# Performance work log

Measured on AMD Instinct MI355X. Metric: run time of the kernel, lower is better.

The kernel has to match this reference:

```python
import jax, jax.numpy as jnp
import numpy as np

B, S, E, H, D, RD = 1, 2048, 2560, 32, 80, 32  # batch, seq, n_embd, heads, head_dim, rotary_dim


def setup_inputs() -> dict:
    key = jax.random.key(0)
    k0, k1, k2 = jax.random.split(key, 3)
    hidden_states = jax.random.normal(k0, (B, S, E), dtype=jnp.float32)
    Wqkv_w = jax.random.normal(k1, (3 * E, E), dtype=jnp.float32) * 0.02
    Wqkv_b = jnp.zeros((3 * E,), dtype=jnp.float32)
    out_w = jax.random.normal(k2, (E, E), dtype=jnp.float32) * 0.02
    out_b = jnp.zeros((E,), dtype=jnp.float32)
    # RotaryEmbedding tables: inv_freq over even indices of rotary_dim
    inv_freq = 1.0 / (10000.0 ** (jnp.arange(0, RD, 2, dtype=jnp.float32) / RD))  # [RD/2]
    t = jnp.arange(S, dtype=jnp.float32)
    freqs = t[:, None] * inv_freq[None, :]  # [S, RD/2]
    return {
        "hidden_states": hidden_states,
        "Wqkv_w": Wqkv_w,
        "Wqkv_b": Wqkv_b,
        "out_w": out_w,
        "out_b": out_b,
        "cos": jnp.cos(freqs),
        "sin": jnp.sin(freqs),
    }


def _apply_rotary(x, cos, sin):
    # x: [B, S, H, D]; rotate first 2*cos.shape[-1] dims (GPT-NeoX half-split style)
    rd = cos.shape[-1] * 2
    x_rot, x_pass = x[..., :rd], x[..., rd:]
    x1, x2 = jnp.split(x_rot, 2, axis=-1)
    c = cos[None, :, None, :]  # [1, S, 1, rd/2]
    s = sin[None, :, None, :]
    rotated = jnp.concatenate([x1 * c - x2 * s, x1 * s + x2 * c], axis=-1)
    return jnp.concatenate([rotated, x_pass], axis=-1)


def reference(hidden_states, Wqkv_w, Wqkv_b, out_w, out_b, cos, sin):
    b, s, e = hidden_states.shape
    qkv = hidden_states @ Wqkv_w.T + Wqkv_b              # [B, S, 3E]
    qkv = qkv.reshape(b, s, 3, H, D)
    q = _apply_rotary(qkv[:, :, 0], cos[:s], sin[:s])    # [B, S, H, D]
    k = _apply_rotary(qkv[:, :, 1], cos[:s], sin[:s])
    v = qkv[:, :, 2]
    scale = 1.0 / np.sqrt(D).astype(np.float32)
    scores = jnp.einsum("bthd,bshd->bhts", q, k) * scale  # [B, H, S, S]
    causal = jnp.triu(jnp.full((s, s), -10000.0, dtype=scores.dtype), 1)
    scores = scores + causal
    attn = jax.nn.softmax(scores, axis=-1)
    out = jnp.einsum("bhts,bshd->bthd", attn, v).reshape(b, s, H * D)
    return out @ out_w.T + out_b
```

## Files before the change

### kernel.cpp

```cpp
#include <hip/hip_runtime.h>
#include <hip/hip_bf16.h>

typedef __attribute__((ext_vector_type(8))) __bf16 bf16x8;
typedef __attribute__((ext_vector_type(8))) short s16x8;
typedef __attribute__((ext_vector_type(4))) float f32x4;
typedef unsigned short u16;
typedef unsigned int u32;

static __device__ __forceinline__ float bf2f(u16 u) {
  union { unsigned int i; float f; } x;
  x.i = ((unsigned int)u) << 16;
  return x.f;
}
static __device__ __forceinline__ u16 f2bf(float f) {
  __hip_bfloat16 h = __float2bfloat16(f);
  return __builtin_bit_cast(u16, h);
}

__global__ void cvt3_kernel(const float* __restrict__ s0, u16* __restrict__ d0, int n0,
                            const float* __restrict__ s1, u16* __restrict__ d1, int n1,
                            const float* __restrict__ s2, u16* __restrict__ d2, int n2) {
  const int stride = gridDim.x * blockDim.x;
  const int t0 = blockIdx.x * blockDim.x + threadIdx.x;
  for (int i = t0; i < n0; i += stride) {
    float4 f = reinterpret_cast<const float4*>(s0)[i];
    ushort4 u{f2bf(f.x), f2bf(f.y), f2bf(f.z), f2bf(f.w)};
    reinterpret_cast<ushort4*>(d0)[i] = u;
  }
  for (int i = t0; i < n1; i += stride) {
    float4 f = reinterpret_cast<const float4*>(s1)[i];
    ushort4 u{f2bf(f.x), f2bf(f.y), f2bf(f.z), f2bf(f.w)};
    reinterpret_cast<ushort4*>(d1)[i] = u;
  }
  for (int i = t0; i < n2; i += stride) {
    float4 f = reinterpret_cast<const float4*>(s2)[i];
    ushort4 u{f2bf(f.x), f2bf(f.y), f2bf(f.z), f2bf(f.w)};
    reinterpret_cast<ushort4*>(d2)[i] = u;
  }
}

template <typename OUT_T>
__global__ __launch_bounds__(512, 2) void gemm256_bt(
    const u16* __restrict__ A, const u16* __restrict__ B,
    const float* __restrict__ bias, OUT_T* __restrict__ C,
    int M, int N, int K) {
  __shared__ u16 As[2][256 * 64];
  __shared__ u16 Bs[2][256 * 64];
  const int tid = threadIdx.x;
  const int w = tid >> 6;
  const int lane = tid & 63;
  const int g = lane >> 4, c = lane & 15;
  const int wm = w >> 2, wn = w & 3;
  const int nwg = gridDim.x * gridDim.y;
  const int flat = blockIdx.y * gridDim.x + blockIdx.x;
  const int swz = (flat & 7) * (nwg >> 3) + (flat >> 3);
  const int bx = swz % gridDim.x, by = swz / gridDim.x;
  const int row0 = by * 256, col0 = bx * 256;
  const int nt = K >> 6;

  f32x4 acc[8][4] = {};

  auto issue = [&](const u16* __restrict__ base, int rb, int t, u16* lds) {
#pragma unroll
    for (int rr = 0; rr < 4; ++rr) {
      int q = rr * 512 + tid;
      int r = q >> 3;
      int cl = (q & 7) ^ (r & 7);
      const u16* gp = base + (size_t)(rb + r) * K + (t << 6) + cl * 8;
      __builtin_amdgcn_global_load_lds(
          (const __attribute__((address_space(1))) void*)gp,
          (__attribute__((address_space(3))) void*)(lds + q * 8), 16, 0, 0);
    }
  };

  issue(A, row0, 0, As[0]);
  issue(B, col0, 0, Bs[0]);

  int cur = 0;
  for (int t = 0; t < nt; ++t) {
    if (t + 1 < nt) {
      issue(A, row0, t + 1, As[cur ^ 1]);
      issue(B, col0, t + 1, Bs[cur ^ 1]);
      asm volatile("s_waitcnt vmcnt(8)" ::: "memory");
    } else {
      asm volatile("s_waitcnt vmcnt(0)" ::: "memory");
    }
    __builtin_amdgcn_s_barrier();

#pragma unroll
    for (int kk = 0; kk < 2; ++kk) {
      bf16x8 bfr[4], afr[8];
      const int p = (kk * 4 + g) ^ (c & 7);
#pragma unroll
      for (int nf = 0; nf < 4; ++nf) {
        int rowb = wn * 64 + nf * 16 + c;
        bfr[nf] = *reinterpret_cast<const bf16x8*>(&Bs[cur][(rowb * 8 + p) * 8]);
      }
#pragma unroll
      for (int mf = 0; mf < 8; ++mf) {
        int rowa = wm * 128 + mf * 16 + c;
        afr[mf] = *reinterpret_cast<const bf16x8*>(&As[cur][(rowa * 8 + p) * 8]);
      }
      __builtin_amdgcn_s_setprio(1);
#pragma unroll
      for (int mf = 0; mf < 8; ++mf)
#pragma unroll
        for (int nf = 0; nf < 4; ++nf)
          acc[mf][nf] = __builtin_amdgcn_mfma_f32_16x16x32_bf16(
              afr[mf], bfr[nf], acc[mf][nf], 0, 0, 0);
      __builtin_amdgcn_s_setprio(0);
    }
    __builtin_amdgcn_s_barrier();
    cur ^= 1;
  }

#pragma unroll
  for (int mf = 0; mf < 8; ++mf) {
#pragma unroll
    for (int nf = 0; nf < 4; ++nf) {
      int col = col0 + wn * 64 + nf * 16 + c;
      float bs = bias[col];
#pragma unroll
      for (int r = 0; r < 4; ++r) {
        int row = row0 + wm * 128 + mf * 16 + g * 4 + r;
        float v = acc[mf][nf][r] + bs;
        if constexpr (sizeof(OUT_T) == 2) {
          C[(size_t)row * N + col] = f2bf(v);
        } else {
          C[(size_t)row * N + col] = v;
        }
      }
    }
  }
}

template <typename OUT_T>
__global__ __launch_bounds__(256, 2) void gemm128p_bt(
    const u16* __restrict__ A, const u16* __restrict__ B,
    const float* __restrict__ bias, OUT_T* __restrict__ C,
    int M, int N, int K) {
  __shared__ u16 As[2][128 * 64];
  __shared__ u16 Bs[2][128 * 64];
  const int tid = threadIdx.x;
  const int w = tid >> 6;
  const int lane = tid & 63;
  const int g = lane >> 4, c = lane & 15;
  const int wm = w >> 1, wn = w & 1;
  const int nwg = gridDim.x * gridDim.y;
  const int flat = blockIdx.y * gridDim.x + blockIdx.x;
  const int swz = (flat & 7) * (nwg >> 3) + (flat >> 3);
  const int bx = swz % gridDim.x, by = swz / gridDim.x;
  const int row0 = by * 128, col0 = bx * 128;
  const int nt = K >> 6;

  f32x4 acc[4][4] = {};

  auto issue = [&](const u16* __restrict__ base, int rb, int t, u16* lds) {
#pragma unroll
    for (int rr = 0; rr < 4; ++rr) {
      int q = rr * 256 + tid;
      int r = q >> 3;
      int cl = (q & 7) ^ (r & 7);
      const u16* gp = base + (size_t)(rb + r) * K + (t << 6) + cl * 8;
      __builtin_amdgcn_global_load_lds(
          (const __attribute__((address_space(1))) void*)gp,
          (__attribute__((address_space(3))) void*)(lds + q * 8), 16, 0, 0);
    }
  };

  issue(A, row0, 0, As[0]);
  issue(B, col0, 0, Bs[0]);

  int cur = 0;
  for (int t = 0; t < nt; ++t) {
    if (t + 1 < nt) {
      issue(A, row0, t + 1, As[cur ^ 1]);
      issue(B, col0, t + 1, Bs[cur ^ 1]);
      asm volatile("s_waitcnt vmcnt(8)" ::: "memory");
    } else {
      asm volatile("s_waitcnt vmcnt(0)" ::: "memory");
    }
    __builtin_amdgcn_s_barrier();

#pragma unroll
    for (int kk = 0; kk < 2; ++kk) {
      bf16x8 afr[4], bfr[4];
      const int p = (kk * 4 + g) ^ (c & 7);
#pragma unroll
      for (int mi = 0; mi < 4; ++mi) {
        int rowa = wm * 64 + mi * 16 + c;
        afr[mi] = *reinterpret_cast<const bf16x8*>(&As[cur][(rowa * 8 + p) * 8]);
      }
#pragma unroll
      for (int ni = 0; ni < 4; ++ni) {
        int rowb = wn * 64 + ni * 16 + c;
        bfr[ni] = *reinterpret_cast<const bf16x8*>(&Bs[cur][(rowb * 8 + p) * 8]);
      }
      __builtin_amdgcn_s_setprio(1);
#pragma unroll
      for (int mi = 0; mi < 4; ++mi)
#pragma unroll
        for (int ni = 0; ni < 4; ++ni)
          acc[mi][ni] = __builtin_amdgcn_mfma_f32_16x16x32_bf16(
              afr[mi], bfr[ni], acc[mi][ni], 0, 0, 0);
      __builtin_amdgcn_s_setprio(0);
    }
    __builtin_amdgcn_s_barrier();
    cur ^= 1;
  }

#pragma unroll
  for (int mi = 0; mi < 4; ++mi) {
#pragma unroll
    for (int ni = 0; ni < 4; ++ni) {
      int col = col0 + wn * 64 + ni * 16 + c;
      float bs = bias[col];
#pragma unroll
      for (int r = 0; r < 4; ++r) {
        int row = row0 + wm * 64 + mi * 16 + g * 4 + r;
        float v = acc[mi][ni][r] + bs;
        if constexpr (sizeof(OUT_T) == 2) {
          C[(size_t)row * N + col] = f2bf(v);
        } else {
          C[(size_t)row * N + col] = v;
        }
      }
    }
  }
}

__global__ __launch_bounds__(256) void rope_kernel(
    const u16* __restrict__ qkv, const float* __restrict__ cosT,
    const float* __restrict__ sinT, u16* __restrict__ Qp, u16* __restrict__ Kp) {
  const int h = blockIdx.y;
  const int d = threadIdx.x & 127;
  const int sh = threadIdx.x >> 7;
  const float scale = 0.16129822f;
#pragma unroll
  for (int i = 0; i < 8; ++i) {
    const int s = blockIdx.x * 16 + i * 2 + sh;
    const size_t row = (size_t)s * 7680;
    if (d < 96) {
      float qo = 0.f, ko = 0.f;
      if (d < 80) {
        float q = bf2f(qkv[row + h * 80 + d]);
        float k = bf2f(qkv[row + 2560 + h * 80 + d]);
        if (d < 16) {
          float cs = cosT[s * 16 + d], sn = sinT[s * 16 + d];
          float q2 = bf2f(qkv[row + h * 80 + d + 16]);
          float k2 = bf2f(qkv[row + 2560 + h * 80 + d + 16]);
          qo = q * cs - q2 * sn;
          ko = k * cs - k2 * sn;
        } else if (d < 32) {
          float cs = cosT[s * 16 + d - 16], sn = sinT[s * 16 + d - 16];
          float q1 = bf2f(qkv[row + h * 80 + d - 16]);
          float k1 = bf2f(qkv[row + 2560 + h * 80 + d - 16]);
          qo = q1 * sn + q * cs;
          ko = k1 * sn + k * cs;
        } else {
          qo = q;
          ko = k;
        }
      }
      size_t o = ((size_t)h * 2048 + s) * 96 + d;
      Qp[o] = f2bf(qo * scale);
      Kp[o] = f2bf(ko);
    }
  }
}

__global__ __launch_bounds__(256) void vtrans_kernel(const u16* __restrict__ qkv,
                                                     u16* __restrict__ Vt) {
  __shared__ u16 Vs[80 * 136];
  const int tid = threadIdx.x;
  const int s0 = blockIdx.x * 128;
  const int h = blockIdx.y;
  const int s = tid >> 1;
  const int h2 = tid & 1;
#pragma unroll
  for (int j = 0; j < 5; ++j) {
    s16x8 v = *reinterpret_cast<const s16x8*>(
        &qkv[(size_t)(s0 + s) * 7680 + 5120 + h * 80 + h2 * 40 + j * 8]);
#pragma unroll
    for (int e = 0; e < 8; ++e)
      Vs[(h2 * 40 + j * 8 + e) * 136 + s] = (u16)v[e];
  }
  __syncthreads();
  for (int idx = tid; idx < 80 * 16; idx += 256) {
    int d = idx >> 4, s8 = idx & 15;
    s16x8 v = *reinterpret_cast<const s16x8*>(&Vs[d * 136 + s8 * 8]);
    *reinterpret_cast<s16x8*>(&Vt[((size_t)(h * 80 + d)) * 2048 + s0 + s8 * 8]) = v;
  }
}

__global__ __launch_bounds__(256, 2) void attn_kernel(
    const u16* __restrict__ Qp, const u16* __restrict__ Kp,
    const u16* __restrict__ Vt, u16* __restrict__ O) {
  __shared__ u32 Plds[4][32 * 36];
  __shared__ float mbuf[4][2][16];
  const int tid = threadIdx.x;
  const int w = tid >> 6;
  const int lane = tid & 63;
  const int g = lane >> 4, c = lane & 15;
  const int f = blockIdx.x;
  const int xcd = f & 7;
  const int k_ = f >> 3;
  const int h = (xcd << 2) | (k_ & 3);
  const int qb = 63 - (k_ >> 2);
  const int q0 = qb * 32;
  const size_t hq = (size_t)h * 2048;
  u32* Pw = &Plds[w][0];

  bf16x8 bq[2][3];
#pragma unroll
  for (int qi = 0; qi < 2; ++qi)
#pragma unroll
    for (int ch = 0; ch < 3; ++ch)
      bq[qi][ch] = *reinterpret_cast<const bf16x8*>(
          &Qp[(hq + q0 + qi * 16 + c) * 96 + ch * 32 + g * 8]);

  f32x4 accO[2][5] = {};
  float mrow[2] = {-1e30f, -1e30f};
  float lrow[2] = {0.f, 0.f};

  const int nkb = (q0 + 95) >> 6;
  for (int kbi = w; kbi < nkb; kbi += 4) {
    const int kb = kbi << 6;
    bf16x8 ak[4][3];
#pragma unroll
    for (int ki = 0; ki < 4; ++ki)
#pragma unroll
      for (int ch = 0; ch < 3; ++ch)
        ak[ki][ch] = *reinterpret_cast<const bf16x8*>(
            &Kp[(hq + kb + ki * 16 + c) * 96 + ch * 32 + g * 8]);
    bf16x8 av[5][2];
#pragma unroll
    for (int db = 0; db < 5; ++db)
#pragma unroll
      for (int kc = 0; kc < 2; ++kc)
        av[db][kc] = *reinterpret_cast<const bf16x8*>(
            &Vt[((size_t)h * 80 + db * 16 + c) * 2048 + kb + kc * 32 + g * 8]);

    f32x4 SS[4][2] = {};
    __builtin_amdgcn_s_setprio(1);
#pragma unroll
    for (int ch = 0; ch < 3; ++ch)
#pragma unroll
      for (int ki = 0; ki < 4; ++ki)
#pragma unroll
        for (int qi = 0; qi < 2; ++qi)
          SS[ki][qi] = __builtin_amdgcn_mfma_f32_16x16x32_bf16(
              ak[ki][ch], bq[qi][ch], SS[ki][qi], 0, 0, 0);
    __builtin_amdgcn_s_setprio(0);

    if (kbi == nkb - 1) {
#pragma unroll
      for (int ki = 0; ki < 4; ++ki)
#pragma unroll
        for (int qi = 0; qi < 2; ++qi)
#pragma unroll
          for (int r = 0; r < 4; ++r) {
            int k = kb + ki * 16 + g * 4 + r;
            int q = q0 + qi * 16 + c;
            if (k > q) SS[ki][qi][r] -= 14426.95f;
          }
    }

    float pmax[2];
    bool need = false;
#pragma unroll
    for (int qi = 0; qi < 2; ++qi) {
      float m2 = SS[0][qi][0];
#pragma unroll
      for (int ki = 0; ki < 4; ++ki)
#pragma unroll
        for (int r = 0; r < 4; ++r)
          if (ki | r) m2 = fmaxf(m2, SS[ki][qi][r]);
      m2 = fmaxf(m2, __shfl_xor(m2, 16));
      m2 = fmaxf(m2, __shfl_xor(m2, 32));
      pmax[qi] = m2;
      need = need || (m2 > mrow[qi] + 8.0f);
    }
    if (__any(need)) {
#pragma unroll
      for (int qi = 0; qi < 2; ++qi) {
        float mnew = fmaxf(mrow[qi], pmax[qi]);
        float sc = __builtin_amdgcn_exp2f(mrow[qi] - mnew);
        lrow[qi] *= sc;
#pragma unroll
        for (int db = 0; db < 5; ++db) accO[qi][db] *= sc;
        mrow[qi] = mnew;
      }
    }
#pragma unroll
    for (int qi = 0; qi < 2; ++qi) {
      float rs = 0.f;
#pragma unroll
      for (int ki = 0; ki < 4; ++ki)
#pragma unroll
        for (int r = 0; r < 4; ++r) {
          float pv = __builtin_amdgcn_exp2f(SS[ki][qi][r] - mrow[qi]);
          SS[ki][qi][r] = pv;
          rs += pv;
        }
      rs += __shfl_xor(rs, 16);
      rs += __shfl_xor(rs, 32);
      lrow[qi] += rs;
    }

#pragma unroll
    for (int qi = 0; qi < 2; ++qi)
#pragma unroll
      for (int ki = 0; ki < 4; ++ki)
#pragma unroll
        for (int r2 = 0; r2 < 2; ++r2) {
          u32 lo = f2bf(SS[ki][qi][r2 * 2]);
          u32 hi = f2bf(SS[ki][qi][r2 * 2 + 1]);
          Pw[(qi * 16 + c) * 36 + ki * 8 + g * 2 + r2] = lo | (hi << 16);
        }
    bf16x8 pa[2][2];
#pragma unroll
    for (int qi = 0; qi < 2; ++qi)
#pragma unroll
      for (int kc = 0; kc < 2; ++kc)
        pa[qi][kc] = *reinterpret_cast<const bf16x8*>(
            &Pw[(qi * 16 + c) * 36 + kc * 16 + g * 4]);

    __builtin_amdgcn_s_setprio(1);
#pragma unroll
    for (int kc = 0; kc < 2; ++kc)
#pragma unroll
      for (int db = 0; db < 5; ++db)
#pragma unroll
        for (int qi = 0; qi < 2; ++qi)
          accO[qi][db] = __builtin_amdgcn_mfma_f32_16x16x32_bf16(
              av[db][kc], pa[qi][kc], accO[qi][db], 0, 0, 0);
    __builtin_amdgcn_s_setprio(0);
  }

  mbuf[w][0][c] = mrow[0];
  mbuf[w][1][c] = mrow[1];
  __syncthreads();
#pragma unroll
  for (int qi = 0; qi < 2; ++qi) {
    float ms = fmaxf(fmaxf(mbuf[0][qi][c], mbuf[1][qi][c]),
                     fmaxf(mbuf[2][qi][c], mbuf[3][qi][c]));
    float fl = __builtin_amdgcn_exp2f(mrow[qi] - ms);
    lrow[qi] *= fl;
#pragma unroll
    for (int db = 0; db < 5; ++db) accO[qi][db] *= fl;
  }
  float* mg = (float*)&Plds[0][0] + lane * 44;
  if (w == 0) {
#pragma unroll
    for (int qi = 0; qi < 2; ++qi)
#pragma unroll
      for (int db = 0; db < 5; ++db)
        *reinterpret_cast<f32x4*>(mg + (qi * 5 + db) * 4) = accO[qi][db];
    mg[40] = lrow[0];
    mg[41] = lrow[1];
  }
  __syncthreads();
  if (w == 1) {
#pragma unroll
    for (int qi = 0; qi < 2; ++qi)
#pragma unroll
      for (int db = 0; db < 5; ++db) {
        f32x4 t = *reinterpret_cast<f32x4*>(mg + (qi * 5 + db) * 4);
        *reinterpret_cast<f32x4*>(mg + (qi * 5 + db) * 4) = t + accO[qi][db];
      }
    mg[40] += lrow[0];
    mg[41] += lrow[1];
  }
  __syncthreads();
  if (w == 2) {
#pragma unroll
    for (int qi = 0; qi < 2; ++qi)
#pragma unroll
      for (int db = 0; db < 5; ++db) {
        f32x4 t = *reinterpret_cast<f32x4*>(mg + (qi * 5 + db) * 4);
        *reinterpret_cast<f32x4*>(mg + (qi * 5 + db) * 4) = t + accO[qi][db];
      }
    mg[40] += lrow[0];
    mg[41] += lrow[1];
  }
  __syncthreads();
  if (w == 3) {
    float lf[2];
    lf[0] = 1.0f / (mg[40] + lrow[0]);
    lf[1] = 1.0f / (mg[41] + lrow[1]);
#pragma unroll
    for (int qi = 0; qi < 2; ++qi)
#pragma unroll
      for (int db = 0; db < 5; ++db) {
        f32x4 t = *reinterpret_cast<f32x4*>(mg + (qi * 5 + db) * 4);
        t = t + accO[qi][db];
        ushort4 o4;
        o4.x = f2bf(t[0] * lf[qi]);
        o4.y = f2bf(t[1] * lf[qi]);
        o4.z = f2bf(t[2] * lf[qi]);
        o4.w = f2bf(t[3] * lf[qi]);
        *reinterpret_cast<ushort4*>(
            &O[(size_t)(q0 + qi * 16 + c) * 2560 + h * 80 + db * 16 + g * 4]) = o4;
      }
  }
}

extern "C" void kernel_launch(void* const* d_in, const int* in_sizes, int n_in,
                              void* d_out, int out_size, void* d_ws, size_t ws_size,
                              hipStream_t stream) {
  const float* hs = (const float*)d_in[0];
  const float* Wqkv_w = (const float*)d_in[1];
  const float* Wqkv_b = (const float*)d_in[2];
  const float* out_w = (const float*)d_in[3];
  const float* out_b = (const float*)d_in[4];
  const float* cosT = (const float*)d_in[5];
  const float* sinT = (const float*)d_in[6];
  float* out = (float*)d_out;

  u16* ws = (u16*)d_ws;
  u16* hsb = ws;
  u16* wqkvb = hsb + (size_t)2048 * 2560;
  u16* outwb = wqkvb + (size_t)7680 * 2560;
  u16* qkv = outwb + (size_t)2560 * 2560;
  u16* Qp = qkv + (size_t)2048 * 7680;
  u16* Kp = Qp + (size_t)32 * 2048 * 96;
  u16* Vt = Kp + (size_t)32 * 2048 * 96;
  u16* attn = qkv;

  cvt3_kernel<<<dim3(2048), dim3(256), 0, stream>>>(
      hs, hsb, 5242880 / 4, Wqkv_w, wqkvb, 19660800 / 4, out_w, outwb, 6553600 / 4);

  gemm256_bt<u16><<<dim3(30, 8), dim3(512), 0, stream>>>(hsb, wqkvb, Wqkv_b, qkv,
                                                         2048, 7680, 2560);
  rope_kernel<<<dim3(128, 32), dim3(256), 0, stream>>>(qkv, cosT, sinT, Qp, Kp);
  vtrans_kernel<<<dim3(16, 32), dim3(256), 0, stream>>>(qkv, Vt);
  attn_kernel<<<dim3(2048), dim3(256), 0, stream>>>(Qp, Kp, Vt, attn);
  gemm128p_bt<float><<<dim3(20, 16), dim3(256), 0, stream>>>(attn, outwb, out_b, out,
                                                             2048, 2560, 2560);
}
```

Measured before the change: 257.5 us.

## Retile QKV GEMM to 128x256 blocks with K32 steps and higher occupancy

Replaces the 256x256 tile, K=64 QKV projection GEMM with a 128x256 tile, K=32 variant. The LDS swizzle and load pattern are reworked for the narrower K slice, and launch bounds now allow four blocks per CU. This doubles the grid from 240 to 480 blocks so the large CU count on the device is better filled, at the cost of less operand reuse per block and more barriers per unit of K. Separately, the output-projection GEMM's end-of-step barrier is moved inside its inner kk loop, which adds synchronisation.

Result: no change. 257.2 us (-0.1%).

```diff
diff --git a/kernel.cpp b/kernel.cpp
--- a/kernel.cpp
+++ b/kernel.cpp
@@ -40,12 +40,12 @@
 }
 
 template <typename OUT_T>
-__global__ __launch_bounds__(512, 2) void gemm256_bt(
+__global__ __launch_bounds__(512, 4) void gemm128x256_bt(
     const u16* __restrict__ A, const u16* __restrict__ B,
     const float* __restrict__ bias, OUT_T* __restrict__ C,
     int M, int N, int K) {
-  __shared__ u16 As[2][256 * 64];
-  __shared__ u16 Bs[2][256 * 64];
+  __shared__ u16 As[2][128 * 32];
+  __shared__ u16 Bs[2][256 * 32];
   const int tid = threadIdx.x;
   const int w = tid >> 6;
   const int lane = tid & 63;
@@ -55,75 +55,82 @@
   const int flat = blockIdx.y * gridDim.x + blockIdx.x;
   const int swz = (flat & 7) * (nwg >> 3) + (flat >> 3);
   const int bx = swz % gridDim.x, by = swz / gridDim.x;
-  const int row0 = by * 256, col0 = bx * 256;
-  const int nt = K >> 6;
-
-  f32x4 acc[8][4] = {};
-
-  auto issue = [&](const u16* __restrict__ base, int rb, int t, u16* lds) {
-#pragma unroll
-    for (int rr = 0; rr < 4; ++rr) {
+  const int row0 = by * 128, col0 = bx * 256;
+  const int nt = K >> 5;
+
+  f32x4 acc[4][4] = {};
+
+  auto issueA = [&](int t, u16* lds) {
+    int q = tid;
+    int r = q >> 2;
+    int cl = (q & 3) ^ ((r >> 1) & 3);
+    const u16* gp = A + (size_t)(row0 + r) * K + (t << 5) + cl * 8;
+    __builtin_amdgcn_global_load_lds(
+        (const __attribute__((address_space(1))) void*)gp,
+        (__attribute__((address_space(3))) void*)(lds + q * 8), 16, 0, 0);
+  };
+  auto issueB = [&](int t, u16* lds) {
+#pragma unroll
+    for (int rr = 0; rr < 2; ++rr) {
       int q = rr * 512 + tid;
-      int r = q >> 3;
-      int cl = (q & 7) ^ (r & 7);
-      const u16* gp = base + (size_t)(rb + r) * K + (t << 6) + cl * 8;
+      int r = q >> 2;
+      int cl = (q & 3) ^ ((r >> 1) & 3);
+      const u16* gp = B + (size_t)(col0 + r) * K + (t << 5) + cl * 8;
       __builtin_amdgcn_global_load_lds(
           (const __attribute__((address_space(1))) void*)gp,
           (__attribute__((address_space(3))) void*)(lds + q * 8), 16, 0, 0);
     }
   };
 
-  issue(A, row0, 0, As[0]);
-  issue(B, col0, 0, Bs[0]);
+  issueA(0, As[0]);
+  issueB(0, Bs[0]);
 
   int cur = 0;
   for (int t = 0; t < nt; ++t) {
     if (t + 1 < nt) {
-      issue(A, row0, t + 1, As[cur ^ 1]);
-      issue(B, col0, t + 1, Bs[cur ^ 1]);
-      asm volatile("s_waitcnt vmcnt(8)" ::: "memory");
+      issueA(t + 1, As[cur ^ 1]);
+      issueB(t + 1, Bs[cur ^ 1]);
+      asm volatile("s_waitcnt vmcnt(3)" ::: "memory");
     } else {
       asm volatile("s_waitcnt vmcnt(0)" ::: "memory");
     }
     __builtin_amdgcn_s_barrier();
 
-#pragma unroll
-    for (int kk = 0; kk < 2; ++kk) {
-      bf16x8 bfr[4], afr[8];
-      const int p = (kk * 4 + g) ^ (c & 7);
-#pragma unroll
-      for (int nf = 0; nf < 4; ++nf) {
-        int rowb = wn * 64 + nf * 16 + c;
-        bfr[nf] = *reinterpret_cast<const bf16x8*>(&Bs[cur][(rowb * 8 + p) * 8]);
-      }
-#pragma unroll
-      for (int mf = 0; mf < 8; ++mf) {
-        int rowa = wm * 128 + mf * 16 + c;
-        afr[mf] = *reinterpret_cast<const bf16x8*>(&As[cur][(rowa * 8 + p) * 8]);
-      }
-      __builtin_amdgcn_s_setprio(1);
-#pragma unroll
-      for (int mf = 0; mf < 8; ++mf)
-#pragma unroll
-        for (int nf = 0; nf < 4; ++nf)
-          acc[mf][nf] = __builtin_amdgcn_mfma_f32_16x16x32_bf16(
-              afr[mf], bfr[nf], acc[mf][nf], 0, 0, 0);
-      __builtin_amdgcn_s_setprio(0);
-    }
+    bf16x8 afr[4], bfr[4];
+#pragma unroll
+    for (int mi = 0; mi < 4; ++mi) {
+      int rowa = wm * 64 + mi * 16 + c;
+      int p = g ^ ((rowa >> 1) & 3);
+      afr[mi] = *reinterpret_cast<const bf16x8*>(&As[cur][(rowa * 4 + p) * 8]);
+    }
+#pragma unroll
+    for (int ni = 0; ni < 4; ++ni) {
+      int rowb = wn * 64 + ni * 16 + c;
+      int p = g ^ ((rowb >> 1) & 3);
+      bfr[ni] = *reinterpret_cast<const bf16x8*>(&Bs[cur][(rowb * 4 + p) * 8]);
+    }
+    __builtin_amdgcn_s_setprio(1);
+#pragma unroll
+    for (int mi = 0; mi < 4; ++mi)
+#pragma unroll
+      for (int ni = 0; ni < 4; ++ni)
+        acc[mi][ni] = __builtin_amdgcn_mfma_f32_16x16x32_bf16(
+            afr[mi], bfr[ni], acc[mi][ni], 0, 0, 0);
+    __builtin_amdgcn_s_setprio(0);
     __builtin_amdgcn_s_barrier();
     cur ^= 1;
   }
 
 #pragma unroll
-  for (int mf = 0; mf < 8; ++mf) {
-#pragma unroll
-    for (int nf = 0; nf < 4; ++nf) {
-      int col = col0 + wn * 64 + nf * 16 + c;
+  for (int mi = 0; mi < 4; ++mi) {
+#pragma unroll
+    for (int ni = 0; ni < 4; ++ni) {
+      int col = col0 + wn * 64 + ni * 16 + c;
       float bs = bias[col];
 #pragma unroll
       for (int r = 0; r < 4; ++r) {
-        int row = row0 + wm * 128 + mf * 16 + g * 4 + r;
-        float v = acc[mf][nf][r] + bs;
+        int row = row0 + wm * 64 + mi * 16 + g * 4 + r;
+        float v = acc[mi][ni][r] + bs;
         if constexpr (sizeof(OUT_T) == 2) {
           C[(size_t)row * N + col] = f2bf(v);
         } else {
@@ -204,8 +211,8 @@
           acc[mi][ni] = __builtin_amdgcn_mfma_f32_16x16x32_bf16(
               afr[mi], bfr[ni], acc[mi][ni], 0, 0, 0);
       __builtin_amdgcn_s_setprio(0);
-    }
-    __builtin_amdgcn_s_barrier();
+      __builtin_amdgcn_s_barrier();
+    }
     cur ^= 1;
   }
 
@@ -531,8 +538,8 @@
   cvt3_kernel<<<dim3(2048), dim3(256), 0, stream>>>(
       hs, hsb, 5242880 / 4, Wqkv_w, wqkvb, 19660800 / 4, out_w, outwb, 6553600 / 4);
 
-  gemm256_bt<u16><<<dim3(30, 8), dim3(512), 0, stream>>>(hsb, wqkvb, Wqkv_b, qkv,
-                                                         2048, 7680, 2560);
+  gemm128x256_bt<u16><<<dim3(30, 16), dim3(512), 0, stream>>>(
+      hsb, wqkvb, Wqkv_b, qkv, 2048, 7680, 2560);
   rope_kernel<<<dim3(128, 32), dim3(256), 0, stream>>>(qkv, cosT, sinT, Qp, Kp);
   vtrans_kernel<<<dim3(16, 32), dim3(256), 0, stream>>>(qkv, Vt);
   attn_kernel<<<dim3(2048), dim3(256), 0, stream>>>(Qp, Kp, Vt, attn);
```
